# Kernel optimization log

Hardware: AMD Instinct MI355X
Metric: run time of the kernel (lower is better)

Reference implementation:

```python
import jax, jax.numpy as jnp
import numpy as np

DIM = 256
HEADS = 4
HEAD_DIM = DIM // HEADS
MLP_HIDDEN = DIM * 3
B, N = 8, 4096
EPS = 1e-5


def setup_inputs() -> dict:
    key = jax.random.key(0)
    ks = jax.random.split(key, 8)
    s = 0.02
    return {
        "x": jax.random.normal(ks[0], (B, N, DIM), dtype=jnp.float32),
        "w_qkv": jax.random.normal(ks[1], (DIM, 3 * DIM), dtype=jnp.float32) * s,
        "b_qkv": jnp.zeros((3 * DIM,), dtype=jnp.float32),
        "norm_g": jnp.ones((DIM,), dtype=jnp.float32),
        "norm_b": jnp.zeros((DIM,), dtype=jnp.float32),
        "w_fc1": jax.random.normal(ks[2], (DIM, MLP_HIDDEN), dtype=jnp.float32) * s,
        "b_fc1": jnp.zeros((MLP_HIDDEN,), dtype=jnp.float32),
        "w_fc2": jax.random.normal(ks[3], (MLP_HIDDEN, DIM), dtype=jnp.float32) * s,
        "b_fc2": jnp.zeros((DIM,), dtype=jnp.float32),
    }


def _layernorm(x, g, b):
    mu = jnp.mean(x, axis=-1, keepdims=True)
    var = jnp.mean(jnp.square(x - mu), axis=-1, keepdims=True)
    return (x - mu) * jax.lax.rsqrt(var + EPS) * g + b


def reference(x, w_qkv, b_qkv, norm_g, norm_b, w_fc1, b_fc1, w_fc2, b_fc2):
    Bx, Nx, C = x.shape
    scale = HEAD_DIM ** -0.5
    qkv = (x @ w_qkv + b_qkv).reshape(Bx, Nx, 3, HEADS, HEAD_DIM)
    qkv = jnp.transpose(qkv, (2, 0, 3, 1, 4))  # [3, B, H, N, hd]
    q, k, v = qkv[0], qkv[1], qkv[2]
    k = k * scale
    # channel attention: [B,H,hd,hd]
    attn = jnp.einsum('bhnd,bhne->bhde', k, v)
    attn = jax.nn.softmax(attn, axis=-1)
    # x_feature[b,h,n,d] = sum_e attn[b,h,d,e] * q[b,h,n,e]
    xf = jnp.einsum('bhde,bhne->bhnd', attn, q)
    xf = jnp.transpose(xf, (0, 2, 1, 3)).reshape(Bx, Nx, C)
    x = x + xf
    # FFN with residual (exact GELU as torch nn.GELU default)
    h = _layernorm(x, norm_g, norm_b)
    h = jax.nn.gelu(h @ w_fc1 + b_fc1, approximate=False) @ w_fc2 + b_fc2
    return x + h
```

## Files before the change

### kernel.cpp

```cpp
#include <hip/hip_runtime.h>
#include <math.h>

typedef __bf16 bf16_t;
typedef __bf16 bf16x4 __attribute__((ext_vector_type(4)));
typedef __bf16 bf16x8 __attribute__((ext_vector_type(8)));
typedef float f32x4 __attribute__((ext_vector_type(4)));

#define DIMC 256
#define HID 768
#define NB 8
#define NN 4096
#define ROWS (NB*NN)
#define NCHUNK 32

#define AS1 __attribute__((address_space(1)))
#define AS3 __attribute__((address_space(3)))

__device__ __forceinline__ void gll16(const bf16_t* src, void* lds) {
  __builtin_amdgcn_global_load_lds((const AS1 void*)src, (AS3 void*)lds, 16, 0, 0);
}

__device__ __forceinline__ float gelu_exact(float v) {
  return 0.5f * v * (1.0f + erff(v * 0.70710678118654752f));
}

__device__ __forceinline__ void pack_w_body(int idx, const float* __restrict__ w,
                                            bf16_t* __restrict__ out, int K, int Nw) {
  int lane = idx & 63;
  int kq = (idx >> 6) % (K >> 5);
  int nt = idx / ((K >> 5) << 6);
  int n = nt * 16 + (lane & 15);
  int k0 = kq * 32 + (lane >> 4) * 8;
  bf16x8 o;
#pragma unroll
  for (int j = 0; j < 8; ++j) o[j] = (bf16_t)w[(size_t)(k0 + j) * Nw + n];
  *(bf16x8*)(out + (size_t)idx * 8) = o;
}

__global__ __launch_bounds__(256)
void prep_all_kernel(const float* __restrict__ x, bf16_t* __restrict__ xb,
                     const float* __restrict__ w_qkv, bf16_t* __restrict__ Bq,
                     const float* __restrict__ w_fc1, bf16_t* __restrict__ B1,
                     const float* __restrict__ w_fc2, bf16_t* __restrict__ B2) {
  const int bid = blockIdx.x, tid = threadIdx.x;
  if (bid < 4096) {
    int i = (bid * 256 + tid) * 8;
    f32x4 a = *(const f32x4*)(x + i);
    f32x4 b = *(const f32x4*)(x + i + 4);
    bf16x8 o;
    o[0] = (bf16_t)a[0]; o[1] = (bf16_t)a[1]; o[2] = (bf16_t)a[2]; o[3] = (bf16_t)a[3];
    o[4] = (bf16_t)b[0]; o[5] = (bf16_t)b[1]; o[6] = (bf16_t)b[2]; o[7] = (bf16_t)b[3];
    *(bf16x8*)(xb + i) = o;
  } else if (bid < 4192) {
    pack_w_body((bid - 4096) * 256 + tid, w_qkv, Bq, 256, 768);
  } else if (bid < 4288) {
    pack_w_body((bid - 4192) * 256 + tid, w_fc1, B1, 256, 768);
  } else {
    pack_w_body((bid - 4288) * 256 + tid, w_fc2, B2, 768, 256);
  }
}

template <int EPI>
__global__ __launch_bounds__(256, 2)
void gemm_packed_kernel(const bf16_t* __restrict__ A, const bf16_t* __restrict__ Bp,
                        const float* __restrict__ bias, bf16_t* __restrict__ outp) {
  __shared__ __align__(16) unsigned char smem[32768];
  const int tid = threadIdx.x;
  const int d = blockIdx.x + blockIdx.y * 4;
  const int w_ = (d & 7) * 256 + (d >> 3);
  const int panel = w_ & 3, rowb = w_ >> 2;
  const int m0 = rowb * 64;
  const int n0 = panel * 192;
  const int lane = tid & 63, w = tid >> 6;
  const int lr = lane & 15, lk = lane >> 4;

#pragma unroll
  for (int i = 0; i < 8; ++i) {
    int idx = i * 256 + tid;
    int row = idx >> 5, pk = idx & 31;
    gll16(A + (size_t)(m0 + row) * 256 + ((pk ^ (row & 7)) * 8), smem + idx * 16);
  }
  asm volatile("s_waitcnt vmcnt(0)" ::: "memory");
  __builtin_amdgcn_s_barrier();

  f32x4 acc[4][3] = {};
  const bf16_t* bb = Bp + (size_t)((panel * 12 + w * 3) * 8) * 512 + lane * 8;

  bf16x8 bf[3][3];
  bf16x8 af[2][4];
#pragma unroll
  for (int nf = 0; nf < 3; ++nf) {
    bf[0][nf] = *(const bf16x8*)(bb + (nf * 8 + 0) * 512);
    bf[1][nf] = *(const bf16x8*)(bb + (nf * 8 + 1) * 512);
  }
#pragma unroll
  for (int mi = 0; mi < 4; ++mi) {
    int row = mi * 16 + lr;
    af[0][mi] = *(const bf16x8*)(smem + row * 512 + ((lk ^ (row & 7)) * 16));
  }

#pragma unroll
  for (int kq = 0; kq < 8; ++kq) {
    if (kq < 6) {
#pragma unroll
      for (int nf = 0; nf < 3; ++nf)
        bf[(kq + 2) % 3][nf] = *(const bf16x8*)(bb + (nf * 8 + kq + 2) * 512);
    }
    if (kq < 7) {
#pragma unroll
      for (int mi = 0; mi < 4; ++mi) {
        int row = mi * 16 + lr;
        af[(kq + 1) & 1][mi] =
            *(const bf16x8*)(smem + row * 512 + ((((kq + 1) * 4 + lk) ^ (row & 7)) * 16));
      }
    }
    __builtin_amdgcn_s_setprio(1);
#pragma unroll
    for (int nf = 0; nf < 3; ++nf)
#pragma unroll
      for (int mi = 0; mi < 4; ++mi)
        acc[mi][nf] = __builtin_amdgcn_mfma_f32_16x16x32_bf16(bf[kq % 3][nf], af[kq & 1][mi],
                                                              acc[mi][nf], 0, 0, 0);
    __builtin_amdgcn_s_setprio(0);
  }

  f32x4 bs[3];
#pragma unroll
  for (int nf = 0; nf < 3; ++nf)
    bs[nf] = *(const f32x4*)(bias + n0 + w * 48 + nf * 16 + lk * 4);

  __syncthreads();
#pragma unroll
  for (int mi = 0; mi < 4; ++mi) {
    int row_l = mi * 16 + lr;
#pragma unroll
    for (int nf = 0; nf < 3; ++nf) {
      int col = w * 48 + nf * 16 + lk * 4;
      f32x4 v = acc[mi][nf] + bs[nf];
      bf16x4 o;
#pragma unroll
      for (int r = 0; r < 4; ++r) {
        float val = v[r];
        if (EPI == 1) val = gelu_exact(val);
        o[r] = (bf16_t)val;
      }
      int chunk = col >> 3;
      int half = (col >> 2) & 1;
      *(bf16x4*)(smem + row_l * 384 + ((chunk ^ (row_l & 7)) << 4) + (half << 3)) = o;
    }
  }
  __syncthreads();
#pragma unroll
  for (int i = 0; i < 6; ++i) {
    int id = i * 256 + tid;
    int row_l = id / 24, c = id % 24;
    bf16x8 v = *(const bf16x8*)(smem + row_l * 384 + ((c ^ (row_l & 7)) << 4));
    *(bf16x8*)(outp + (size_t)(m0 + row_l) * 768 + n0 + c * 8) = v;
  }
}

__global__ __launch_bounds__(256, 2)
void fc2_packed_kernel(const bf16_t* __restrict__ mid, const bf16_t* __restrict__ Bp,
                       const float* __restrict__ bias, const bf16_t* __restrict__ resid,
                       float* __restrict__ outp) {
  __shared__ __align__(16) unsigned char smem[2 * 16384 + 32768];
  unsigned char* epi = smem + 32768;
  const int tid = threadIdx.x;
  const int m0 = blockIdx.x * 64;
  const int lane = tid & 63, w = tid >> 6;
  const int lr = lane & 15, lk = lane >> 4;

  auto stageA = [&](int c, int buf) {
#pragma unroll
    for (int i = 0; i < 4; ++i) {
      int idx = i * 256 + tid;
      int row = idx >> 4, pk = idx & 15;
      gll16(mid + (size_t)(m0 + row) * 768 + c * 128 + ((pk ^ (row & 7)) * 8),
            smem + buf * 16384 + idx * 16);
    }
  };

  stageA(0, 0);
  stageA(1, 1);
  asm volatile("s_waitcnt vmcnt(4)" ::: "memory");
  __builtin_amdgcn_s_barrier();

  f32x4 acc[4][4] = {};
#pragma unroll
  for (int c = 0; c < 6; ++c) {
    bf16x8 bf[4][4];
#pragma unroll
    for (int nf = 0; nf < 4; ++nf)
#pragma unroll
      for (int kql = 0; kql < 4; ++kql)
        bf[nf][kql] = *(const bf16x8*)(Bp + (size_t)((w * 4 + nf) * 24 + c * 4 + kql) * 512 + lane * 8);
    asm volatile("s_waitcnt vmcnt(0)" ::: "memory");
    __builtin_amdgcn_s_barrier();
#pragma unroll
    for (int kql = 0; kql < 4; ++kql) {
#pragma unroll
      for (int mi = 0; mi < 4; ++mi) {
        int row = mi * 16 + lr;
        bf16x8 a8 = *(const bf16x8*)(smem + (c & 1) * 16384 + row * 256 +
                                     (((kql * 4 + lk) ^ (row & 7)) * 16));
#pragma unroll
        for (int nf = 0; nf < 4; ++nf)
          acc[mi][nf] = __builtin_amdgcn_mfma_f32_16x16x32_bf16(bf[nf][kql], a8, acc[mi][nf], 0, 0, 0);
      }
    }
    __builtin_amdgcn_s_barrier();
    if (c + 2 < 6) stageA(c + 2, c & 1);
  }

  f32x4 bs[4];
#pragma unroll
  for (int nf = 0; nf < 4; ++nf)
    bs[nf] = *(const f32x4*)(bias + w * 64 + nf * 16 + lk * 4);

#pragma unroll
  for (int ph = 0; ph < 2; ++ph) {
    if (ph == 1) __syncthreads();
#pragma unroll
    for (int mj = 0; mj < 2; ++mj) {
      int mi = ph * 2 + mj;
      int row_l = mj * 16 + lr;
#pragma unroll
      for (int nf = 0; nf < 4; ++nf) {
        int cc = w * 64 + nf * 16 + lk * 4;
        f32x4 v = acc[mi][nf] + bs[nf];
        int chunk = cc >> 2;
        *(f32x4*)(epi + row_l * 1024 + ((chunk ^ (row_l & 7)) << 4)) = v;
      }
    }
    __syncthreads();
#pragma unroll
    for (int i = 0; i < 8; ++i) {
      int id = i * 256 + tid;
      int rl = id >> 6, c = id & 63;
      f32x4 v = *(const f32x4*)(epi + rl * 1024 + ((c ^ (rl & 7)) << 4));
      int grow = m0 + ph * 32 + rl;
      bf16x4 rz = *(const bf16x4*)(resid + (size_t)grow * 256 + c * 4);
#pragma unroll
      for (int r = 0; r < 4; ++r) v[r] += (float)rz[r];
      *(f32x4*)(outp + (size_t)grow * 256 + c * 4) = v;
    }
  }
}

__global__ __launch_bounds__(256)
void attn_kv_kernel(const bf16_t* __restrict__ qkv, float* __restrict__ part) {
  const int bh = blockIdx.x, chunk = blockIdx.y;
  const int b = bh >> 2, h = bh & 3;
  __shared__ __align__(16) float kl[32][68];
  __shared__ __align__(16) float vl[32][68];
  const int tid = threadIdx.x;
  const int dg = tid >> 4, eg = tid & 15;
  f32x4 acc[4] = {};
  const int n00 = chunk * (NN / NCHUNK);
  const int srow = tid >> 3, spk = tid & 7;
  for (int t = 0; t < (NN / NCHUNK) / 32; ++t) {
    int n0 = n00 + t * 32;
    {
      const bf16x8 k8 = *(const bf16x8*)(qkv + (size_t)(b * NN + n0 + srow) * HID + 256 + h * 64 + spk * 8);
      const bf16x8 v8 = *(const bf16x8*)(qkv + (size_t)(b * NN + n0 + srow) * HID + 512 + h * 64 + spk * 8);
#pragma unroll
      for (int j = 0; j < 8; ++j) kl[srow][spk * 8 + j] = (float)k8[j];
#pragma unroll
      for (int j = 0; j < 8; ++j) vl[srow][spk * 8 + j] = (float)v8[j];
    }
    __syncthreads();
#pragma unroll 8
    for (int n = 0; n < 32; ++n) {
      f32x4 k4 = *(const f32x4*)&kl[n][dg * 4];
      f32x4 v4 = *(const f32x4*)&vl[n][eg * 4];
#pragma unroll
      for (int i = 0; i < 4; ++i) acc[i] += k4[i] * v4;
    }
    __syncthreads();
  }
  float* dst = part + (size_t)(chunk * 32 + bh) * 4096;
#pragma unroll
  for (int i = 0; i < 4; ++i)
    *(f32x4*)&dst[(dg * 4 + i) * 64 + eg * 4] = acc[i];
}

__global__ __launch_bounds__(256)
void attn_softmax_kernel(const float* __restrict__ part, bf16_t* __restrict__ attnb) {
  const int bh = blockIdx.x;
  const int tid = threadIdx.x;
  const int dg = tid >> 4, eg = tid & 15;
  f32x4 s[4] = {};
  for (int c = 0; c < NCHUNK; ++c) {
    const float* src = part + (size_t)(c * 32 + bh) * 4096;
#pragma unroll
    for (int i = 0; i < 4; ++i) s[i] += *(const f32x4*)&src[(dg * 4 + i) * 64 + eg * 4];
  }
  bf16_t* dst = attnb + (size_t)bh * 4096;
#pragma unroll
  for (int i = 0; i < 4; ++i) {
    f32x4 l = s[i] * 0.125f;
    float m = fmaxf(fmaxf(l[0], l[1]), fmaxf(l[2], l[3]));
#pragma unroll
    for (int msk = 1; msk < 16; msk <<= 1) m = fmaxf(m, __shfl_xor(m, msk));
    f32x4 p;
    float sum = 0.f;
#pragma unroll
    for (int j = 0; j < 4; ++j) { p[j] = expf(l[j] - m); sum += p[j]; }
#pragma unroll
    for (int msk = 1; msk < 16; msk <<= 1) sum += __shfl_xor(sum, msk);
    float inv = 1.0f / sum;
    bf16x4 o;
#pragma unroll
    for (int j = 0; j < 4; ++j) o[j] = (bf16_t)(p[j] * inv);
    *(bf16x4*)&dst[(dg * 4 + i) * 64 + eg * 4] = o;
  }
}

__global__ __launch_bounds__(256, 2)
void xf_ln_mfma_kernel(const bf16_t* __restrict__ qkv, const bf16_t* __restrict__ attnb,
                       const bf16_t* __restrict__ xb, bf16_t* __restrict__ x2b,
                       bf16_t* __restrict__ hln, const float* __restrict__ gamma,
                       const float* __restrict__ beta) {
  __shared__ __align__(16) unsigned char qs[32768];
  __shared__ float red[4][4][16][2];
  const int tid = threadIdx.x;
  const int row0 = blockIdx.x * 64;
  const int b = row0 >> 12;
  const int lane = tid & 63, h = tid >> 6;
  const int lr = lane & 15, lk = lane >> 4;

#pragma unroll
  for (int i = 0; i < 8; ++i) {
    int idx = i * 256 + tid;
    int row = idx >> 5, pk = idx & 31;
    gll16(qkv + (size_t)(row0 + row) * HID + ((pk ^ (row & 7)) * 8), qs + idx * 16);
  }
  asm volatile("s_waitcnt vmcnt(0)" ::: "memory");
  __builtin_amdgcn_s_barrier();

  bf16x8 af[4][2];
#pragma unroll
  for (int mi = 0; mi < 4; ++mi)
#pragma unroll
    for (int kk = 0; kk < 2; ++kk) {
      int row = mi * 16 + lr;
      int pk = h * 8 + kk * 4 + lk;
      af[mi][kk] = *(const bf16x8*)(qs + row * 512 + ((pk ^ (row & 7)) * 16));
    }
  bf16x8 bfr[4][2];
#pragma unroll
  for (int nf = 0; nf < 4; ++nf)
#pragma unroll
    for (int kk = 0; kk < 2; ++kk)
      bfr[nf][kk] = *(const bf16x8*)(attnb + (size_t)(b * 4 + h) * 4096 +
                                     (nf * 16 + lr) * 64 + kk * 32 + lk * 8);
  f32x4 acc[4][4] = {};
#pragma unroll
  for (int kk = 0; kk < 2; ++kk)
#pragma unroll
    for (int mi = 0; mi < 4; ++mi)
#pragma unroll
      for (int nf = 0; nf < 4; ++nf)
        acc[mi][nf] = __builtin_amdgcn_mfma_f32_16x16x32_bf16(bfr[nf][kk], af[mi][kk], acc[mi][nf], 0, 0, 0);

  float ps[4], pq[4];
#pragma unroll
  for (int mi = 0; mi < 4; ++mi) {
    ps[mi] = 0.f; pq[mi] = 0.f;
    int row = row0 + mi * 16 + lr;
#pragma unroll
    for (int nf = 0; nf < 4; ++nf) {
      int col = h * 64 + nf * 16 + lk * 4;
      size_t off = (size_t)row * DIMC + col;
      bf16x4 xv = *(const bf16x4*)(xb + off);
      f32x4 x2;
#pragma unroll
      for (int r = 0; r < 4; ++r) {
        x2[r] = acc[mi][nf][r] + (float)xv[r];
        ps[mi] += x2[r]; pq[mi] += x2[r] * x2[r];
      }
      acc[mi][nf] = x2;
      bf16x4 o;
#pragma unroll
      for (int r = 0; r < 4; ++r) o[r] = (bf16_t)x2[r];
      *(bf16x4*)(x2b + off) = o;
    }
#pragma unroll
    for (int m = 16; m < 64; m <<= 1) {
      ps[mi] += __shfl_xor(ps[mi], m);
      pq[mi] += __shfl_xor(pq[mi], m);
    }
  }
  if (lk == 0) {
#pragma unroll
    for (int mi = 0; mi < 4; ++mi) { red[h][mi][lr][0] = ps[mi]; red[h][mi][lr][1] = pq[mi]; }
  }
  __builtin_amdgcn_s_barrier();
#pragma unroll
  for (int mi = 0; mi < 4; ++mi) {
    float t1 = red[0][mi][lr][0] + red[1][mi][lr][0] + red[2][mi][lr][0] + red[3][mi][lr][0];
    float t2 = red[0][mi][lr][1] + red[1][mi][lr][1] + red[2][mi][lr][1] + red[3][mi][lr][1];
    float mu = t1 * (1.0f / 256.0f);
    float var = t2 * (1.0f / 256.0f) - mu * mu;
    float rs = rsqrtf(var + 1e-5f);
    int row = row0 + mi * 16 + lr;
#pragma unroll
    for (int nf = 0; nf < 4; ++nf) {
      int col = h * 64 + nf * 16 + lk * 4;
      f32x4 g4 = *(const f32x4*)(gamma + col);
      f32x4 b4 = *(const f32x4*)(beta + col);
      bf16x4 o;
#pragma unroll
      for (int r = 0; r < 4; ++r)
        o[r] = (bf16_t)((acc[mi][nf][r] - mu) * rs * g4[r] + b4[r]);
      *(bf16x4*)(hln + (size_t)row * DIMC + col) = o;
    }
  }
}

extern "C" void kernel_launch(void* const* d_in, const int* in_sizes, int n_in,
                              void* d_out, int out_size, void* d_ws, size_t ws_size,
                              hipStream_t stream) {
  const float* x      = (const float*)d_in[0];
  const float* w_qkv  = (const float*)d_in[1];
  const float* b_qkv  = (const float*)d_in[2];
  const float* norm_g = (const float*)d_in[3];
  const float* norm_b = (const float*)d_in[4];
  const float* w_fc1  = (const float*)d_in[5];
  const float* b_fc1  = (const float*)d_in[6];
  const float* w_fc2  = (const float*)d_in[7];
  const float* b_fc2  = (const float*)d_in[8];

  char* ws = (char*)d_ws;
  size_t off = 0;
  bf16_t* qkv   = (bf16_t*)(ws + off); off += (size_t)ROWS * HID * 2;
  bf16_t* mid   = qkv;
  bf16_t* xb    = (bf16_t*)(ws + off); off += (size_t)ROWS * DIMC * 2;
  bf16_t* hln   = (bf16_t*)(ws + off); off += (size_t)ROWS * DIMC * 2;
  bf16_t* x2b   = (bf16_t*)(ws + off); off += (size_t)ROWS * DIMC * 2;
  float*  part  = (float*)(ws + off);  off += (size_t)NCHUNK * 32 * 4096 * 4;
  bf16_t* attnb = (bf16_t*)(ws + off); off += (size_t)32 * 4096 * 2;
  bf16_t* Bq    = (bf16_t*)(ws + off); off += (size_t)768 * 256 * 2;
  bf16_t* B1    = (bf16_t*)(ws + off); off += (size_t)768 * 256 * 2;
  bf16_t* B2    = (bf16_t*)(ws + off); off += (size_t)256 * 768 * 2;

  prep_all_kernel<<<4384, 256, 0, stream>>>(x, xb, w_qkv, Bq, w_fc1, B1, w_fc2, B2);

  gemm_packed_kernel<0><<<dim3(4, ROWS / 64), 256, 0, stream>>>(xb, Bq, b_qkv, qkv);
  attn_kv_kernel<<<dim3(32, NCHUNK), 256, 0, stream>>>(qkv, part);
  attn_softmax_kernel<<<32, 256, 0, stream>>>(part, attnb);
  xf_ln_mfma_kernel<<<ROWS / 64, 256, 0, stream>>>(qkv, attnb, xb, x2b, hln, norm_g, norm_b);
  gemm_packed_kernel<1><<<dim3(4, ROWS / 64), 256, 0, stream>>>(hln, B1, b_fc1, mid);
  fc2_packed_kernel<<<ROWS / 64, 256, 0, stream>>>(mid, B2, b_fc2, x2b, (float*)d_out);
}
```

Baseline: 125.3 us.

## Keep weight panel in registers and loop four row tiles per block with double-buffered A

The QKV and FC1 GEMM kernels now load their 192-column weight slice into registers once per block and process four 64-row A tiles per block instead of one. A tiles are staged into two LDS buffers with async global-to-LDS loads, and the next tiles are prefetched while the current one computes. The goal is to stop re-reading weights from global memory for every 64-row tile and to overlap A loads with MFMA work. The grid shrinks from 2048 to 512 blocks, and 24 bf16x8 weight registers per thread plus 64 KB of LDS per block raise register and LDS pressure. That may lower occupancy, and the hand-tuned vmcnt counts must match the exact number of outstanding loads.

Result: slower. 129.9 us (+3.7%).

```diff
diff --git a/kernel.cpp b/kernel.cpp
--- a/kernel.cpp
+++ b/kernel.cpp
@@ -62,100 +62,111 @@
 
 template <int EPI>
 __global__ __launch_bounds__(256, 2)
-void gemm_packed_kernel(const bf16_t* __restrict__ A, const bf16_t* __restrict__ Bp,
-                        const float* __restrict__ bias, bf16_t* __restrict__ outp) {
-  __shared__ __align__(16) unsigned char smem[32768];
+void gemm_bres_kernel(const bf16_t* __restrict__ A, const bf16_t* __restrict__ Bp,
+                      const float* __restrict__ bias, bf16_t* __restrict__ outp) {
+  __shared__ __align__(16) unsigned char smem[2][32768];
   const int tid = threadIdx.x;
   const int d = blockIdx.x + blockIdx.y * 4;
-  const int w_ = (d & 7) * 256 + (d >> 3);
-  const int panel = w_ & 3, rowb = w_ >> 2;
-  const int m0 = rowb * 64;
+  const int w_ = (d & 7) * 64 + (d >> 3);
+  const int panel = w_ & 3, mgrp = w_ >> 2;
+  const int m0 = mgrp * 256;
   const int n0 = panel * 192;
   const int lane = tid & 63, w = tid >> 6;
   const int lr = lane & 15, lk = lane >> 4;
 
-#pragma unroll
-  for (int i = 0; i < 8; ++i) {
-    int idx = i * 256 + tid;
-    int row = idx >> 5, pk = idx & 31;
-    gll16(A + (size_t)(m0 + row) * 256 + ((pk ^ (row & 7)) * 8), smem + idx * 16);
-  }
-  asm volatile("s_waitcnt vmcnt(0)" ::: "memory");
-  __builtin_amdgcn_s_barrier();
-
-  f32x4 acc[4][3] = {};
   const bf16_t* bb = Bp + (size_t)((panel * 12 + w * 3) * 8) * 512 + lane * 8;
-
-  bf16x8 bf[3][3];
-  bf16x8 af[2][4];
-#pragma unroll
-  for (int nf = 0; nf < 3; ++nf) {
-    bf[0][nf] = *(const bf16x8*)(bb + (nf * 8 + 0) * 512);
-    bf[1][nf] = *(const bf16x8*)(bb + (nf * 8 + 1) * 512);
-  }
-#pragma unroll
-  for (int mi = 0; mi < 4; ++mi) {
-    int row = mi * 16 + lr;
-    af[0][mi] = *(const bf16x8*)(smem + row * 512 + ((lk ^ (row & 7)) * 16));
-  }
-
-#pragma unroll
-  for (int kq = 0; kq < 8; ++kq) {
-    if (kq < 6) {
-#pragma unroll
-      for (int nf = 0; nf < 3; ++nf)
-        bf[(kq + 2) % 3][nf] = *(const bf16x8*)(bb + (nf * 8 + kq + 2) * 512);
-    }
-    if (kq < 7) {
-#pragma unroll
-      for (int mi = 0; mi < 4; ++mi) {
-        int row = mi * 16 + lr;
-        af[(kq + 1) & 1][mi] =
-            *(const bf16x8*)(smem + row * 512 + ((((kq + 1) * 4 + lk) ^ (row & 7)) * 16));
-      }
-    }
-    __builtin_amdgcn_s_setprio(1);
-#pragma unroll
-    for (int nf = 0; nf < 3; ++nf)
-#pragma unroll
-      for (int mi = 0; mi < 4; ++mi)
-        acc[mi][nf] = __builtin_amdgcn_mfma_f32_16x16x32_bf16(bf[kq % 3][nf], af[kq & 1][mi],
-                                                              acc[mi][nf], 0, 0, 0);
-    __builtin_amdgcn_s_setprio(0);
-  }
+  bf16x8 bq[3][8];
+#pragma unroll
+  for (int nf = 0; nf < 3; ++nf)
+#pragma unroll
+    for (int kq = 0; kq < 8; ++kq)
+      bq[nf][kq] = *(const bf16x8*)(bb + (nf * 8 + kq) * 512);
+
+  auto stage = [&](int c, int buf) {
+#pragma unroll
+    for (int i = 0; i < 8; ++i) {
+      int idx = i * 256 + tid;
+      int row = idx >> 5, pk = idx & 31;
+      gll16(A + (size_t)(m0 + c * 64 + row) * 256 + ((pk ^ (row & 7)) * 8),
+            smem[buf] + idx * 16);
+    }
+  };
+  stage(0, 0);
+  stage(1, 1);
 
   f32x4 bs[3];
 #pragma unroll
   for (int nf = 0; nf < 3; ++nf)
     bs[nf] = *(const f32x4*)(bias + n0 + w * 48 + nf * 16 + lk * 4);
 
-  __syncthreads();
-#pragma unroll
-  for (int mi = 0; mi < 4; ++mi) {
-    int row_l = mi * 16 + lr;
-#pragma unroll
-    for (int nf = 0; nf < 3; ++nf) {
-      int col = w * 48 + nf * 16 + lk * 4;
-      f32x4 v = acc[mi][nf] + bs[nf];
-      bf16x4 o;
-#pragma unroll
-      for (int r = 0; r < 4; ++r) {
-        float val = v[r];
-        if (EPI == 1) val = gelu_exact(val);
-        o[r] = (bf16_t)val;
+#pragma unroll
+  for (int c = 0; c < 4; ++c) {
+    if (c == 0)      asm volatile("s_waitcnt vmcnt(8)" ::: "memory");
+    else if (c < 3)  asm volatile("s_waitcnt vmcnt(14)" ::: "memory");
+    else             asm volatile("s_waitcnt vmcnt(6)" ::: "memory");
+    __builtin_amdgcn_s_barrier();
+
+    const unsigned char* ab = smem[c & 1];
+    f32x4 acc[4][3] = {};
+    bf16x8 af[2][4];
+#pragma unroll
+    for (int mi = 0; mi < 4; ++mi) {
+      int row = mi * 16 + lr;
+      af[0][mi] = *(const bf16x8*)(ab + row * 512 + ((lk ^ (row & 7)) * 16));
+    }
+#pragma unroll
+    for (int kq = 0; kq < 8; ++kq) {
+      if (kq < 7) {
+#pragma unroll
+        for (int mi = 0; mi < 4; ++mi) {
+          int row = mi * 16 + lr;
+          af[(kq + 1) & 1][mi] =
+              *(const bf16x8*)(ab + row * 512 + ((((kq + 1) * 4 + lk) ^ (row & 7)) * 16));
+        }
       }
-      int chunk = col >> 3;
-      int half = (col >> 2) & 1;
-      *(bf16x4*)(smem + row_l * 384 + ((chunk ^ (row_l & 7)) << 4) + (half << 3)) = o;
-    }
-  }
-  __syncthreads();
-#pragma unroll
-  for (int i = 0; i < 6; ++i) {
-    int id = i * 256 + tid;
-    int row_l = id / 24, c = id % 24;
-    bf16x8 v = *(const bf16x8*)(smem + row_l * 384 + ((c ^ (row_l & 7)) << 4));
-    *(bf16x8*)(outp + (size_t)(m0 + row_l) * 768 + n0 + c * 8) = v;
+      __builtin_amdgcn_s_setprio(1);
+#pragma unroll
+      for (int nf = 0; nf < 3; ++nf)
+#pragma unroll
+        for (int mi = 0; mi < 4; ++mi)
+          acc[mi][nf] = __builtin_amdgcn_mfma_f32_16x16x32_bf16(bq[nf][kq], af[kq & 1][mi],
+                                                                acc[mi][nf], 0, 0, 0);
+      __builtin_amdgcn_s_setprio(0);
+    }
+    __builtin_amdgcn_s_barrier();
+
+    unsigned char* eb = (unsigned char*)smem[c & 1];
+#pragma unroll
+    for (int mi = 0; mi < 4; ++mi) {
+      int row_l = mi * 16 + lr;
+#pragma unroll
+      for (int nf = 0; nf < 3; ++nf) {
+        int col = w * 48 + nf * 16 + lk * 4;
+        f32x4 v = acc[mi][nf] + bs[nf];
+        bf16x4 o;
+#pragma unroll
+        for (int r = 0; r < 4; ++r) {
+          float val = v[r];
+          if (EPI == 1) val = gelu_exact(val);
+          o[r] = (bf16_t)val;
+        }
+        int chunk = col >> 3;
+        int half = (col >> 2) & 1;
+        *(bf16x4*)(eb + row_l * 384 + ((chunk ^ (row_l & 7)) << 4) + (half << 3)) = o;
+      }
+    }
+    __syncthreads();
+#pragma unroll
+    for (int i = 0; i < 6; ++i) {
+      int id = i * 256 + tid;
+      int row_l = id / 24, cc = id % 24;
+      bf16x8 v = *(const bf16x8*)(eb + row_l * 384 + ((cc ^ (row_l & 7)) << 4));
+      *(bf16x8*)(outp + (size_t)(m0 + c * 64 + row_l) * 768 + n0 + cc * 8) = v;
+    }
+    if (c < 2) {
+      __syncthreads();
+      stage(c + 2, c & 1);
+    }
   }
 }
 
@@ -446,10 +457,10 @@
 
   prep_all_kernel<<<4384, 256, 0, stream>>>(x, xb, w_qkv, Bq, w_fc1, B1, w_fc2, B2);
 
-  gemm_packed_kernel<0><<<dim3(4, ROWS / 64), 256, 0, stream>>>(xb, Bq, b_qkv, qkv);
+  gemm_bres_kernel<0><<<dim3(4, 128), 256, 0, stream>>>(xb, Bq, b_qkv, qkv);
   attn_kv_kernel<<<dim3(32, NCHUNK), 256, 0, stream>>>(qkv, part);
   attn_softmax_kernel<<<32, 256, 0, stream>>>(part, attnb);
   xf_ln_mfma_kernel<<<ROWS / 64, 256, 0, stream>>>(qkv, attnb, xb, x2b, hln, norm_g, norm_b);
-  gemm_packed_kernel<1><<<dim3(4, ROWS / 64), 256, 0, stream>>>(hln, B1, b_fc1, mid);
+  gemm_bres_kernel<1><<<dim3(4, 128), 256, 0, stream>>>(hln, B1, b_fc1, mid);
   fc2_packed_kernel<<<ROWS / 64, 256, 0, stream>>>(mid, B2, b_fc2, x2b, (float*)d_out);
 }
```
